# Performance work log

Hardware: AMD Instinct MI355X
Metric: run time of the kernel (lower is better)

## Reference

```python
import jax, jax.numpy as jnp
import numpy as np

H = 16                 # num_heads
BITS = (2, 4, 8)       # adaptive quantization precision options


def _adaptive_quant(t, labels):
    """t: [B,S,HD], labels: [B,S] int in {0,1,2}. Per-level masked min/max
    affine quantize-dequantize, matching AdaptiveQuantization.forward."""
    out = jnp.zeros_like(t)
    for level, bits in enumerate(BITS):
        m = (labels == level)[..., None]          # [B,S,1] broadcast over features
        qmax = float(2 ** bits - 1)
        tmin = jnp.min(jnp.where(m, t, jnp.inf))
        tmax = jnp.max(jnp.where(m, t, -jnp.inf))
        degen = (~jnp.isfinite(tmin)) | (~jnp.isfinite(tmax)) | (tmax == tmin)
        scale = jnp.where(degen, 1.0, (tmax - tmin) / qmax)
        zp = jnp.where(degen, 0.0, -tmin / scale)
        dq = (jnp.clip(jnp.round(t / scale + zp), 0.0, qmax) - zp) * scale
        out = jnp.where(m, dq, out)
    return out


def _importance(q, k, w_imp, b_imp, pm_f):
    """q,k: [B,H,S,D]; uses head 0 only, as in compute_importance_scores."""
    D = q.shape[-1]
    q0, k0 = q[:, 0], k[:, 0]                     # [B,S,D]
    attn = jax.nn.softmax(jnp.einsum('bsd,btd->bst', q0, k0) / np.sqrt(D), axis=-1)
    prompt_attn = attn @ pm_f                     # [B,S] sum over prompt keys
    bias = q0.mean(axis=1) @ w_imp + b_imp[0]     # [B]
    return prompt_attn + bias[:, None]            # [B,S]


def _split_heads(x, B, S, D):
    return x.reshape(B, S, H, D).transpose(0, 2, 1, 3)  # [B,H,S,D]


def _forward(hidden_states, Wq, Wk, Wv, Wo, w_imp, b_imp, prompt_mask, k_sel):
    B, S, HD = hidden_states.shape
    D = HD // H
    q = _split_heads(hidden_states @ Wq, B, S, D)
    k = _split_heads(hidden_states @ Wk, B, S, D)
    v = _split_heads(hidden_states @ Wv, B, S, D)
    pm_f = prompt_mask.astype(hidden_states.dtype)
    imp = _importance(q, k, w_imp, b_imp, pm_f)   # [B,S]
    # precision labels: >0.7 -> 2 ; 0.3..0.7 -> 1 ; else 0
    labels = jnp.where(imp > 0.7, 2, jnp.where(imp >= 0.3, 1, 0))
    ck = _adaptive_quant(k.transpose(0, 2, 1, 3).reshape(B, S, HD), labels)
    cv = _adaptive_quant(v.transpose(0, 2, 1, 3).reshape(B, S, HD), labels)
    ck = _split_heads(ck, B, S, D)
    cv = _split_heads(cv, B, S, D)
    if k_sel < S:  # top-k token gather along key/value sequence axis
        _, sel = jax.lax.top_k(imp, k_sel)        # [B,k_sel]
        idx = jnp.broadcast_to(sel[:, None, :, None], (B, H, k_sel, D))
        ck = jnp.take_along_axis(ck, idx, axis=2)
        cv = jnp.take_along_axis(cv, idx, axis=2)
    scores = jnp.einsum('bhsd,bhtd->bhst', q, ck) / np.sqrt(D)
    w = jax.nn.softmax(scores, axis=-1)
    out = jnp.einsum('bhst,bhtd->bhsd', w, cv)
    return out.transpose(0, 2, 1, 3).reshape(B, S, HD) @ Wo


def setup_inputs() -> dict:
    key = jax.random.key(0)
    ks = jax.random.split(key, 8)
    B, S, HD, D = 4, 2048, 1024, 64
    wscale = 2.0 / np.sqrt(HD)   # gives importance-softmax logits std ~4
    return {
        'hidden_states': jax.random.normal(ks[0], (B, S, HD), jnp.float32),
        'Wq': jax.random.normal(ks[1], (HD, HD), jnp.float32) * wscale,
        'Wk': jax.random.normal(ks[2], (HD, HD), jnp.float32) * wscale,
        'Wv': jax.random.normal(ks[3], (HD, HD), jnp.float32) * wscale,
        'Wo': jax.random.normal(ks[4], (HD, HD), jnp.float32) * wscale,
        'w_imp': jax.random.normal(ks[5], (D,), jnp.float32) * 0.02,
        'b_imp': jnp.zeros((1,), jnp.float32),
        'prompt_mask': jax.random.randint(ks[6], (S,), 0, 2).astype(bool),
    }


def reference(hidden_states, Wq, Wk, Wv, Wo, w_imp, b_imp, prompt_mask):
    B, S, HD = hidden_states.shape
    D = HD // H
    # pre-pass to get the (data-dependent, but concrete) selection count
    q = _split_heads(hidden_states @ Wq, B, S, D)
    k = _split_heads(hidden_states @ Wk, B, S, D)
    imp = _importance(q, k, w_imp, b_imp, prompt_mask.astype(hidden_states.dtype))
    thr = jnp.quantile(imp, 0.5)
    k_sel = int(jnp.max(jnp.sum(imp >= thr, axis=1)))
    return _forward(hidden_states, Wq, Wk, Wv, Wo, w_imp, b_imp, prompt_mask, k_sel)
```

## Files before the change

kernel.cpp:

```cpp
#include <hip/hip_runtime.h>
#include <hip/hip_bf16.h>
#include <math.h>

#define B_ 4
#define S_ 2048
#define H_ 16
#define D_ 64
#define HD_ 1024
#define NTOK 8192

#define NEGBIG (-3.0e38f)

typedef unsigned short u16;
typedef unsigned int u32;
typedef __attribute__((ext_vector_type(8))) short bf16x8;
typedef __attribute__((ext_vector_type(4))) float f32x4;
typedef __attribute__((ext_vector_type(4))) u16 u16x4;
typedef __attribute__((ext_vector_type(4))) u32 u32x4;

__device__ __forceinline__ float bf2f(u16 x){
  u32 u = ((u32)x) << 16; float f; __builtin_memcpy(&f, &u, 4); return f;
}
__device__ __forceinline__ u16 f2bf(float f){
  u32 u; __builtin_memcpy(&u, &f, 4);
  u32 r = (u + 0x7FFFu + ((u >> 16) & 1u)) >> 16;
  return (u16)r;
}
__device__ __forceinline__ void split3s(float v, u16 &h, u16 &m, u16 &l){
  h = f2bf(v); float r  = v - bf2f(h);
  m = f2bf(r); float r2 = r - bf2f(m);
  l = f2bf(r2);
}
__device__ __forceinline__ u32 fkey(float f){
  u32 u; __builtin_memcpy(&u, &f, 4);
  return (u & 0x80000000u) ? ~u : (u | 0x80000000u);
}
__device__ __forceinline__ float keyf(u32 k){
  u32 u = (k & 0x80000000u) ? (k & 0x7FFFFFFFu) : ~k;
  float f; __builtin_memcpy(&f, &u, 4); return f;
}
__device__ __forceinline__ void gload16(const u16* g, u16* l){
  __builtin_amdgcn_global_load_lds(
      (const __attribute__((address_space(1))) unsigned int*)g,
      (__attribute__((address_space(3))) unsigned int*)l, 16, 0, 0);
}

#define ST_KSEL 0
#define ST_KPAD 1
#define ST_NCK  2
#define ST_VKEY 4
#define ST_TIES 8
#define ST_MM   12
#define ST_BIAS 36

#define OFF_Q0   0ull
#define OFF_K    2097152ull
#define OFF_V    35651584ull
#define OFF_HS   69206016ull
#define OFF_WP   119537664ull
#define OFF_QB   134742016ull
#define OFF_IMP  151519232ull
#define OFF_LAB  151552000ull
#define OFF_SEL  151584768ull
#define OFF_ST   151617536ull
#define WS_NEED  151618560ull

#define WKH_O 0u
#define WKM_O 1048576u
#define WKL_O 2097152u
#define WVH_O 3145728u
#define WVM_O 4194304u
#define WVL_O 5242880u
#define WQH_O 6291456u
#define WQM_O 7340032u
#define WQL_O 7471104u
#define HSPL  8388608u

__global__ __launch_bounds__(256) void kt_split_h(const float* __restrict__ hid,
    u16* __restrict__ p0, u16* __restrict__ p1, u16* __restrict__ p2, u32* __restrict__ st){
  if (blockIdx.x == 0 && threadIdx.x < 12)
    st[ST_MM + threadIdx.x] = ((threadIdx.x % 6) < 3) ? 0xFFFFFFFFu : 0u;
  size_t i = (size_t)blockIdx.x*256 + threadIdx.x;
  float4 x = ((const float4*)hid)[i];
  u16 a0,a1,a2, b0,b1,b2, c0,c1,c2, d0,d1,d2;
  split3s(x.x, a0,a1,a2);
  split3s(x.y, b0,b1,b2);
  split3s(x.z, c0,c1,c2);
  split3s(x.w, d0,d1,d2);
  u16x4 v0 = {a0,b0,c0,d0};
  u16x4 v1 = {a1,b1,c1,d1};
  u16x4 v2 = {a2,b2,c2,d2};
  ((u16x4*)p0)[i] = v0;
  ((u16x4*)p1)[i] = v1;
  ((u16x4*)p2)[i] = v2;
}

__global__ __launch_bounds__(256) void kt_twts3(const float* __restrict__ Wk,
    const float* __restrict__ Wv, const float* __restrict__ Wq, u16* __restrict__ WP){
  int z = blockIdx.z;
  const float* Win = (z==0) ? Wk : (z==1) ? Wv : Wq;
  u16* wh = WP + ((z==0) ? WKH_O : (z==1) ? WVH_O : WQH_O);
  u16* wm = WP + ((z==0) ? WKM_O : (z==1) ? WVM_O : WQM_O);
  u16* wl = WP + ((z==0) ? WKL_O : (z==1) ? WVL_O : WQL_O);
  int mlrows = (z==2) ? 128 : 1024;
  __shared__ float t[32][33];
  int bx = blockIdx.x*32, by = blockIdx.y*32;
  int tx = threadIdx.x, ty = threadIdx.y;
  #pragma unroll
  for (int i=0;i<32;i+=8) t[ty+i][tx] = Win[(size_t)(by+ty+i)*HD_ + bx+tx];
  __syncthreads();
  #pragma unroll
  for (int i=0;i<32;i+=8){
    float v = t[tx][ty+i];
    int orow = bx+ty+i;
    u16 h,m,l;
    split3s(v,h,m,l);
    wh[(size_t)orow*HD_ + by+tx] = h;
    if (orow < mlrows){
      wm[(size_t)orow*HD_ + by+tx] = m;
      wl[(size_t)orow*HD_ + by+tx] = l;
    }
  }
}

__global__ __launch_bounds__(256) void kt_twto(const float* __restrict__ Win, u16* __restrict__ Wt){
  __shared__ float t[32][33];
  int bx = blockIdx.x*32, by = blockIdx.y*32;
  int tx = threadIdx.x, ty = threadIdx.y;
  #pragma unroll
  for (int i=0;i<32;i+=8) t[ty+i][tx] = Win[(size_t)(by+ty+i)*HD_ + bx+tx];
  __syncthreads();
  #pragma unroll
  for (int i=0;i<32;i+=8) Wt[(size_t)(bx+ty+i)*HD_ + by+tx] = f2bf(t[tx][ty+i]);
}

__global__ __launch_bounds__(256) void kt_gemm_kv1(const u16* __restrict__ HS,
    const u16* __restrict__ B0, const u16* __restrict__ B1, const u16* __restrict__ B2,
    float* __restrict__ Cf){
  int lin = blockIdx.x + (blockIdx.y << 3);
  int nl  = (lin & 7) * 64 + (lin >> 3);
  const int bx = nl & 7, by = nl >> 3;
  __shared__ u16 As0[128*32], As1[128*32], As2[128*32];
  __shared__ u16 Bs0[128*32], Bs1[128*32], Bs2[128*32];
  const int tid = threadIdx.x, lane = tid & 63;
  const int wid = tid >> 6, wr = wid >> 1, wc = wid & 1;
  const int m0 = by * 128, n0 = bx * 128;
  const int srow = lane & 15;
  const int sq   = (lane >> 4) << 3;
  const u16* gp[12];
  u16* lp[12];
  #pragma unroll
  for (int i = 0; i < 12; i++){
    int t = wid + 4*i, pl = t >> 3, g = t & 7;
    int row = g*16 + srow;
    const u16* base = (pl==0)? HS : (pl==1)? HS+HSPL : (pl==2)? HS+2u*HSPL
                     : (pl==3)? B0 : (pl==4)? B1 : B2;
    size_t roff = (pl < 3) ? (size_t)(m0+row)*HD_ : (size_t)(n0+row)*HD_;
    gp[i] = base + roff + sq;
    u16* lb = (pl==0)?As0:(pl==1)?As1:(pl==2)?As2:(pl==3)?Bs0:(pl==4)?Bs1:Bs2;
    lp[i] = lb + g*512;
  }
  f32x4 acc[4][4];
  #pragma unroll
  for (int i=0;i<4;i++)
    #pragma unroll
    for (int j=0;j<4;j++) acc[i][j] = (f32x4){0.f,0.f,0.f,0.f};
  for (int k0 = 0; k0 < HD_; k0 += 32){
    #pragma unroll
    for (int i = 0; i < 12; i++){ gload16(gp[i], lp[i]); gp[i] += 32; }
    __syncthreads();
    const int lro = lane*8;
    bf16x8 a0[4], a1[4], a2[4];
    #pragma unroll
    for (int i=0;i<4;i++){
      int ro = (wr*4 + i)*512 + lro;
      a0[i] = *(const bf16x8*)(As0 + ro);
      a1[i] = *(const bf16x8*)(As1 + ro);
      a2[i] = *(const bf16x8*)(As2 + ro);
    }
    #pragma unroll
    for (int j=0;j<4;j++){
      int co = (wc*4 + j)*512 + lro;
      bf16x8 b0 = *(const bf16x8*)(Bs0 + co);
      bf16x8 b1 = *(const bf16x8*)(Bs1 + co);
      bf16x8 b2 = *(const bf16x8*)(Bs2 + co);
      #pragma unroll
      for (int i=0;i<4;i++){
        acc[i][j] = __builtin_amdgcn_mfma_f32_16x16x32_bf16(a0[i], b0, acc[i][j], 0, 0, 0);
        acc[i][j] = __builtin_amdgcn_mfma_f32_16x16x32_bf16(a1[i], b0, acc[i][j], 0, 0, 0);
        acc[i][j] = __builtin_amdgcn_mfma_f32_16x16x32_bf16(a0[i], b1, acc[i][j], 0, 0, 0);
        acc[i][j] = __builtin_amdgcn_mfma_f32_16x16x32_bf16(a1[i], b1, acc[i][j], 0, 0, 0);
        acc[i][j] = __builtin_amdgcn_mfma_f32_16x16x32_bf16(a2[i], b0, acc[i][j], 0, 0, 0);
        acc[i][j] = __builtin_amdgcn_mfma_f32_16x16x32_bf16(a0[i], b2, acc[i][j], 0, 0, 0);
      }
    }
    __syncthreads();
  }
  const int row0 = m0 + wr*64, col0 = n0 + wc*64;
  #pragma unroll
  for (int i=0;i<4;i++)
    #pragma unroll
    for (int j=0;j<4;j++){
      int rr = row0 + i*16 + ((lane>>4)<<2);
      int cc = col0 + j*16 + (lane&15);
      #pragma unroll
      for (int r=0;r<4;r++)
        Cf[(size_t)(rr+r)*HD_ + cc] = acc[i][j][r];
    }
}

__global__ __launch_bounds__(256) void kt_gemm_q(const u16* __restrict__ HS, const u16* __restrict__ WP,
    u16* __restrict__ qb, float* __restrict__ q0){
  int lin = blockIdx.x + (blockIdx.y << 3);
  int nl  = (lin & 7) * 64 + (lin >> 3);
  const int bx = nl & 7, by = nl >> 3;
  const u16* B0 = WP+WQH_O;
  const u16* B1 = WP+WQM_O;
  const u16* B2 = WP+WQL_O;
  const bool full = (bx == 0);
  __shared__ u16 As0[128*32], As1[128*32], As2[128*32];
  __shared__ u16 Bs0[128*32], Bs1[128*32], Bs2[128*32];
  const int tid = threadIdx.x, lane = tid & 63;
  const int wid = tid >> 6, wr = wid >> 1, wc = wid & 1;
  const int m0 = by * 128, n0 = bx * 128;
  const int srow = lane & 15;
  const int sq   = (lane >> 4) << 3;
  const u16* gp[12];
  u16* lp[12];
  if (full){
    #pragma unroll
    for (int i = 0; i < 12; i++){
      int t = wid + 4*i, pl = t >> 3, g = t & 7;
      int row = g*16 + srow;
      const u16* base = (pl==0)? HS : (pl==1)? HS+HSPL : (pl==2)? HS+2u*HSPL
                       : (pl==3)? B0 : (pl==4)? B1 : B2;
      size_t roff = (pl < 3) ? (size_t)(m0+row)*HD_ : (size_t)(n0+row)*HD_;
      gp[i] = base + roff + sq;
      u16* lb = (pl==0)?As0:(pl==1)?As1:(pl==2)?As2:(pl==3)?Bs0:(pl==4)?Bs1:Bs2;
      lp[i] = lb + g*512;
    }
  } else {
    #pragma unroll
    for (int i = 0; i < 6; i++){
      int t = wid + 4*i, p3 = t >> 3, g = t & 7;
      int pl = (p3 == 2) ? 3 : p3;
      int row = g*16 + srow;
      const u16* base = (pl==0)? HS : (pl==1)? HS+HSPL : B0;
      size_t roff = (pl < 3) ? (size_t)(m0+row)*HD_ : (size_t)(n0+row)*HD_;
      gp[i] = base + roff + sq;
      u16* lb = (pl==0)?As0:(pl==1)?As1:Bs0;
      lp[i] = lb + g*512;
    }
  }
  f32x4 acc[4][4];
  #pragma unroll
  for (int i=0;i<4;i++)
    #pragma unroll
    for (int j=0;j<4;j++) acc[i][j] = (f32x4){0.f,0.f,0.f,0.f};
  for (int k0 = 0; k0 < HD_; k0 += 32){
    if (full){
      #pragma unroll
      for (int i = 0; i < 12; i++){ gload16(gp[i], lp[i]); gp[i] += 32; }
    } else {
      #pragma unroll
      for (int i = 0; i < 6; i++){ gload16(gp[i], lp[i]); gp[i] += 32; }
    }
    __syncthreads();
    const int lro = lane*8;
    bf16x8 a0[4], a1[4], a2[4];
    #pragma unroll
    for (int i=0;i<4;i++){
      int ro = (wr*4 + i)*512 + lro;
      a0[i] = *(const bf16x8*)(As0 + ro);
      a1[i] = *(const bf16x8*)(As1 + ro);
      if (full) a2[i] = *(const bf16x8*)(As2 + ro);
    }
    #pragma unroll
    for (int j=0;j<4;j++){
      int co = (wc*4 + j)*512 + lro;
      bf16x8 b0 = *(const bf16x8*)(Bs0 + co);
      if (full){
        bf16x8 b1 = *(const bf16x8*)(Bs1 + co);
        bf16x8 b2 = *(const bf16x8*)(Bs2 + co);
        #pragma unroll
        for (int i=0;i<4;i++){
          acc[i][j] = __builtin_amdgcn_mfma_f32_16x16x32_bf16(a0[i], b0, acc[i][j], 0, 0, 0);
          acc[i][j] = __builtin_amdgcn_mfma_f32_16x16x32_bf16(a1[i], b0, acc[i][j], 0, 0, 0);
          acc[i][j] = __builtin_amdgcn_mfma_f32_16x16x32_bf16(a0[i], b1, acc[i][j], 0, 0, 0);
          acc[i][j] = __builtin_amdgcn_mfma_f32_16x16x32_bf16(a1[i], b1, acc[i][j], 0, 0, 0);
          acc[i][j] = __builtin_amdgcn_mfma_f32_16x16x32_bf16(a2[i], b0, acc[i][j], 0, 0, 0);
          acc[i][j] = __builtin_amdgcn_mfma_f32_16x16x32_bf16(a0[i], b2, acc[i][j], 0, 0, 0);
        }
      } else {
        #pragma unroll
        for (int i=0;i<4;i++){
          acc[i][j] = __builtin_amdgcn_mfma_f32_16x16x32_bf16(a0[i], b0, acc[i][j], 0, 0, 0);
          acc[i][j] = __builtin_amdgcn_mfma_f32_16x16x32_bf16(a1[i], b0, acc[i][j], 0, 0, 0);
        }
      }
    }
    __syncthreads();
  }
  const int row0 = m0 + wr*64, col0 = n0 + wc*64;
  #pragma unroll
  for (int i=0;i<4;i++)
    #pragma unroll
    for (int j=0;j<4;j++){
      int rr = row0 + i*16 + ((lane>>4)<<2);
      int cc = col0 + j*16 + (lane&15);
      #pragma unroll
      for (int r=0;r<4;r++){
        float v = acc[i][j][r];
        qb[(size_t)(rr+r)*HD_ + cc] = f2bf(v);
        if (cc < 64) q0[(size_t)(rr+r)*64 + cc] = v;
      }
    }
}

__global__ __launch_bounds__(256) void kt_gemm_o(const u16* __restrict__ A, const u16* __restrict__ Bt,
    float* __restrict__ out){
  int lin = blockIdx.x + (blockIdx.y << 3);
  int nl  = (lin & 7) * 64 + (lin >> 3);
  const int bx = nl & 7, by = nl >> 3;
  __shared__ u16 As[128*32];
  __shared__ u16 Bs[128*32];
  const int tid = threadIdx.x, lane = tid & 63;
  const int wid = tid >> 6, wr = wid >> 1, wc = wid & 1;
  const int m0 = by * 128, n0 = bx * 128;
  const u16* gp[4];
  u16* lp[4];
  #pragma unroll
  for (int i = 0; i < 4; i++){
    int t = wid + 4*i, pl = t >> 3, g = t & 7;
    int row = g*16 + (lane & 15);
    gp[i] = (pl ? (Bt + (size_t)(n0+row)*HD_) : (A + (size_t)(m0+row)*HD_)) + ((lane>>4)<<3);
    lp[i] = (pl ? Bs : As) + g*512;
  }
  f32x4 acc[4][4];
  #pragma unroll
  for (int i=0;i<4;i++)
    #pragma unroll
    for (int j=0;j<4;j++) acc[i][j] = (f32x4){0.f,0.f,0.f,0.f};
  for (int k0 = 0; k0 < HD_; k0 += 32){
    #pragma unroll
    for (int i = 0; i < 4; i++){ gload16(gp[i], lp[i]); gp[i] += 32; }
    __syncthreads();
    const int lro = lane*8;
    bf16x8 af[4], bg[4];
    #pragma unroll
    for (int i=0;i<4;i++){
      af[i] = *(const bf16x8*)(As + (wr*4 + i)*512 + lro);
      bg[i] = *(const bf16x8*)(Bs + (wc*4 + i)*512 + lro);
    }
    #pragma unroll
    for (int i=0;i<4;i++)
      #pragma unroll
      for (int j=0;j<4;j++)
        acc[i][j] = __builtin_amdgcn_mfma_f32_16x16x32_bf16(af[i], bg[j], acc[i][j], 0, 0, 0);
    __syncthreads();
  }
  const int row0 = m0 + wr*64, col0 = n0 + wc*64;
  #pragma unroll
  for (int i=0;i<4;i++)
    #pragma unroll
    for (int j=0;j<4;j++){
      int rr = row0 + i*16 + ((lane>>4)<<2);
      int cc = col0 + j*16 + (lane&15);
      #pragma unroll
      for (int r=0;r<4;r++)
        out[(size_t)(rr+r)*HD_ + cc] = acc[i][j][r];
    }
}

__global__ __launch_bounds__(256) void kt_k0t(const float* __restrict__ Kf, float* __restrict__ k0t){
  __shared__ float t[32][33];
  int b = blockIdx.z, s0 = blockIdx.x*32, d0 = blockIdx.y*32;
  int tx = threadIdx.x, ty = threadIdx.y;
  #pragma unroll
  for (int i=0;i<32;i+=8) t[ty+i][tx] = Kf[((size_t)b*S_ + s0+ty+i)*HD_ + d0+tx];
  __syncthreads();
  #pragma unroll
  for (int i=0;i<32;i+=8) k0t[((size_t)b*D_ + d0+ty+i)*S_ + s0+tx] = t[tx][ty+i];
}

__global__ __launch_bounds__(1024) void kt_bias(const float* __restrict__ q0, const float* __restrict__ wimp,
    const float* __restrict__ bimp, u32* __restrict__ st){
  int b = blockIdx.x;
  int d = threadIdx.x & 63, sg = threadIdx.x >> 6;
  float acc = 0.f;
  for (int s = sg; s < S_; s += 16) acc += q0[((size_t)b*S_ + s)*64 + d];
  __shared__ float red[16][64];
  red[sg][d] = acc;
  __syncthreads();
  if (sg == 0){
    float tot = 0.f;
    #pragma unroll
    for (int i=0;i<16;i++) tot += red[i][d];
    float term = (tot / (float)S_) * wimp[d];
    #pragma unroll
    for (int off=32; off; off>>=1) term += __shfl_xor(term, off);
    if (d == 0) ((float*)st)[ST_BIAS + b] = term + bimp[0];
  }
}

__global__ __launch_bounds__(256) void kt_imp(const float* __restrict__ q0, const float* __restrict__ k0t,
    const int* __restrict__ pm, const u32* __restrict__ st, float* __restrict__ imp){
  int b = blockIdx.y, r0 = blockIdx.x * 16;
  int tid = threadIdx.x, lane = tid & 63, w = tid >> 6;
  __shared__ float qs[16][64];
  __shared__ float pms[S_];
  __shared__ int mode8;
  if (tid == 0) mode8 = 0;
  __syncthreads();
  const unsigned char* pmb = (const unsigned char*)pm;
  int flag = 0;
  for (int i = tid; i < S_; i += 256) if (i & 3) flag |= pmb[i];
  if (flag) atomicOr(&mode8, 1);
  for (int i = tid; i < 16*64; i += 256){
    int rr = i >> 6, dd = i & 63;
    qs[rr][dd] = q0[((size_t)b*S_ + r0 + rr)*64 + dd];
  }
  __syncthreads();
  if (mode8){ for (int i = tid; i < S_; i += 256) pms[i] = pmb[i] ? 1.f : 0.f; }
  else      { for (int i = tid; i < S_; i += 256) pms[i] = pm[i]  ? 1.f : 0.f; }
  __syncthreads();
  float sc[4][32];
  #pragma unroll
  for (int r=0;r<4;r++)
    #pragma unroll
    for (int j=0;j<32;j++) sc[r][j] = 0.f;
  const float* kb = k0t + (size_t)b*D_*S_;
  for (int d=0; d<64; d++){
    const float* krow = kb + (size_t)d*S_;
    float kx[32];
    #pragma unroll
    for (int j=0;j<32;j++) kx[j] = krow[lane + 64*j];
    #pragma unroll
    for (int r=0;r<4;r++){
      float qd = qs[w*4 + r][d];
      #pragma unroll
      for (int j=0;j<32;j++) sc[r][j] = fmaf(qd, kx[j], sc[r][j]);
    }
  }
  float bias = ((const float*)st)[ST_BIAS + b];
  #pragma unroll
  for (int r=0;r<4;r++){
    float mx = NEGBIG;
    #pragma unroll
    for (int j=0;j<32;j++) mx = fmaxf(mx, sc[r][j]);
    #pragma unroll
    for (int off=32; off; off>>=1) mx = fmaxf(mx, __shfl_xor(mx, off));
    mx *= 0.125f;
    float se = 0.f, sp = 0.f;
    #pragma unroll
    for (int j=0;j<32;j++){
      float e = expf(sc[r][j]*0.125f - mx);
      se += e;
      sp += e * pms[lane + 64*j];
    }
    #pragma unroll
    for (int off=32; off; off>>=1){ se += __shfl_xor(se, off); sp += __shfl_xor(sp, off); }
    if (lane == 0) imp[(size_t)b*S_ + r0 + w*4 + r] = sp/se + bias;
  }
}

__global__ __launch_bounds__(1024) void kt_stats(const float* __restrict__ imp, u32* __restrict__ st){
  __shared__ u32 keys[NTOK];
  __shared__ u32 res2[2];
  __shared__ int cnts[4];
  int tid = threadIdx.x, lane = tid & 63, w = tid >> 6;
  for (int i = tid; i < NTOK; i += 1024) keys[i] = fkey(imp[i]);
  __syncthreads();
  if (w < 2){
    int kk = 4095 + w;
    u32 lo = 0u, hi = 0xFFFFFFFFu;
    while (lo < hi){
      u32 mid = lo + ((hi - lo) >> 1);
      int c = 0;
      for (int i = lane; i < NTOK; i += 64) c += (keys[i] <= mid) ? 1 : 0;
      #pragma unroll
      for (int off=32; off; off>>=1) c += __shfl_xor(c, off);
      if (c >= kk + 1) hi = mid; else lo = mid + 1;
    }
    if (lane == 0) res2[w] = lo;
  }
  __syncthreads();
  float a = keyf(res2[0]), bq = keyf(res2[1]);
  float thr = __fadd_rn(a, __fmul_rn(__fsub_rn(bq, a), 0.5f));
  u32 tkey = fkey(thr);
  if (w < 4){
    int c = 0;
    for (int i = lane; i < S_; i += 64) c += (keys[w*S_ + i] >= tkey) ? 1 : 0;
    #pragma unroll
    for (int off=32; off; off>>=1) c += __shfl_xor(c, off);
    if (lane == 0) cnts[w] = c;
  }
  __syncthreads();
  int ksel = max(max(cnts[0], cnts[1]), max(cnts[2], cnts[3]));
  if (tid == 0){
    int kpad = (ksel + 63) & ~63;
    ((int*)st)[ST_KSEL] = ksel;
    ((int*)st)[ST_KPAD] = kpad;
    ((int*)st)[ST_NCK]  = kpad >> 6;
  }
  if (w < 4){
    int kk = S_ - ksel;
    u32 lo = 0u, hi = 0xFFFFFFFFu;
    while (lo < hi){
      u32 mid = lo + ((hi - lo) >> 1);
      int c = 0;
      for (int i = lane; i < S_; i += 64) c += (keys[w*S_ + i] <= mid) ? 1 : 0;
      #pragma unroll
      for (int off=32; off; off>>=1) c += __shfl_xor(c, off);
      if (c >= kk + 1) hi = mid; else lo = mid + 1;
    }
    int cle = 0;
    for (int i = lane; i < S_; i += 64) cle += (keys[w*S_ + i] <= lo) ? 1 : 0;
    #pragma unroll
    for (int off=32; off; off>>=1) cle += __shfl_xor(cle, off);
    if (lane == 0){
      st[ST_VKEY + w] = lo;
      ((int*)st)[ST_TIES + w] = ksel - (S_ - cle);
    }
  }
}

__global__ __launch_bounds__(1024) void kt_select(const float* __restrict__ imp, const u32* __restrict__ st,
    int* __restrict__ sel, u32* __restrict__ lab){
  int b = blockIdx.x, tid = threadIdx.x, lane = tid & 63, w = tid >> 6;
  u32 vkey = st[ST_VKEY + b];
  int ties = ((const int*)st)[ST_TIES + b];
  int s0 = tid*2, s1 = s0 + 1;
  float f0 = imp[(size_t)b*S_ + s0], f1 = imp[(size_t)b*S_ + s1];
  lab[(size_t)b*S_ + s0] = (f0 > 0.7f) ? 2u : ((f0 >= 0.3f) ? 1u : 0u);
  lab[(size_t)b*S_ + s1] = (f1 > 0.7f) ? 2u : ((f1 >= 0.3f) ? 1u : 0u);
  u32 k0 = fkey(f0), k1 = fkey(f1);
  int g0 = (k0 > vkey), g1 = (k1 > vkey);
  int t0 = (k0 == vkey), t1 = (k1 == vkey);
  __shared__ int wtot[16];
  int tsum = t0 + t1, incl = tsum;
  #pragma unroll
  for (int off=1; off<64; off<<=1){ int nv = __shfl_up(incl, off); if (lane >= off) incl += nv; }
  if (lane == 63) wtot[w] = incl;
  __syncthreads();
  int woff = 0;
  for (int i=0;i<w;i++) woff += wtot[i];
  int tie0 = woff + incl - tsum;
  int tie1 = tie0 + t0;
  int sf0 = g0 | (t0 & ((tie0 < ties) ? 1 : 0));
  int sf1 = g1 | (t1 & ((tie1 < ties) ? 1 : 0));
  __syncthreads();
  int ssum = sf0 + sf1; incl = ssum;
  #pragma unroll
  for (int off=1; off<64; off<<=1){ int nv = __shfl_up(incl, off); if (lane >= off) incl += nv; }
  if (lane == 63) wtot[w] = incl;
  __syncthreads();
  woff = 0;
  for (int i=0;i<w;i++) woff += wtot[i];
  int p0 = woff + incl - ssum;
  if (sf0) sel[(size_t)b*S_ + p0] = s0;
  if (sf1) sel[(size_t)b*S_ + p0 + sf0] = s1;
}

__global__ __launch_bounds__(256) void kt_minmax(const float* __restrict__ Kf, const float* __restrict__ Vf,
    const u32* __restrict__ lab, u32* __restrict__ st){
  u32 mn[6], mx[6];
  #pragma unroll
  for (int q=0;q<6;q++){ mn[q] = 0xFFFFFFFFu; mx[q] = 0u; }
  const int n4 = NTOK * HD_ / 4;
  for (int i = blockIdx.x*blockDim.x + threadIdx.x; i < n4; i += gridDim.x*blockDim.x){
    u32 l = min(lab[i >> 8], 2u);
    float4 kv = ((const float4*)Kf)[i];
    float4 vv = ((const float4*)Vf)[i];
    u32 a0=fkey(kv.x), a1=fkey(kv.y), a2=fkey(kv.z), a3=fkey(kv.w);
    u32 klo = min(min(a0,a1),min(a2,a3)), khi = max(max(a0,a1),max(a2,a3));
    if (klo < mn[l]) mn[l] = klo;
    if (khi > mx[l]) mx[l] = khi;
    u32 b0=fkey(vv.x), b1=fkey(vv.y), b2=fkey(vv.z), b3=fkey(vv.w);
    u32 vlo = min(min(b0,b1),min(b2,b3)), vhi = max(max(b0,b1),max(b2,b3));
    if (vlo < mn[3+l]) mn[3+l] = vlo;
    if (vhi > mx[3+l]) mx[3+l] = vhi;
  }
  #pragma unroll
  for (int q=0;q<6;q++){
    #pragma unroll
    for (int off=32; off; off>>=1){
      u32 om = (u32)__shfl_xor((int)mn[q], off); if (om < mn[q]) mn[q] = om;
      u32 oM = (u32)__shfl_xor((int)mx[q], off); if (oM > mx[q]) mx[q] = oM;
    }
  }
  __shared__ u32 smn[4][6], smx[4][6];
  int lane = threadIdx.x & 63, w = threadIdx.x >> 6;
  if (lane == 0){
    #pragma unroll
    for (int q=0;q<6;q++){ smn[w][q]=mn[q]; smx[w][q]=mx[q]; }
  }
  __syncthreads();
  if (threadIdx.x < 6){
    int q = threadIdx.x;
    u32 m = smn[0][q], M = smx[0][q];
    #pragma unroll
    for (int i=1;i<4;i++){ if (smn[i][q] < m) m = smn[i][q]; if (smx[i][q] > M) M = smx[i][q]; }
    int minSlot = ST_MM + ((q < 3) ? q : q + 3);
    atomicMin(&st[minSlot], m);
    atomicMax(&st[minSlot + 3], M);
  }
}

__device__ __forceinline__ void scales_for(const u32* st, u32 l, float &qmx,
    float &sK, float &zK, float &sV, float &zV){
  qmx = (l==0) ? 3.f : (l==1) ? 15.f : 255.f;
  u32 mnk = st[ST_MM + l], mxk = st[ST_MM + 3 + l];
  sK = 1.f; zK = 0.f;
  if (!(mnk == 0xFFFFFFFFu || mxk == 0u)){
    float tmn = keyf(mnk), tmx = keyf(mxk);
    if (tmx != tmn){ sK = __fdiv_rn(__fsub_rn(tmx, tmn), qmx); zK = __fdiv_rn(-tmn, sK); }
  }
  u32 mnv = st[ST_MM + 6 + l], mxv = st[ST_MM + 9 + l];
  sV = 1.f; zV = 0.f;
  if (!(mnv == 0xFFFFFFFFu || mxv == 0u)){
    float tmn = keyf(mnv), tmx = keyf(mxv);
    if (tmx != tmn){ sV = __fdiv_rn(__fsub_rn(tmx, tmn), qmx); zV = __fdiv_rn(-tmn, sV); }
  }
}

__device__ __forceinline__ float dqz(float x, float s, float z, float q){
  float t = rintf(__fadd_rn(__fdiv_rn(x, s), z));
  t = fminf(fmaxf(t, 0.f), q);
  return __fmul_rn(__fsub_rn(t, z), s);
}

__global__ __launch_bounds__(256) void kt_buildck(const float* __restrict__ Kf, const float* __restrict__ Vf,
    const int* __restrict__ sel, const u32* __restrict__ lab, const u32* __restrict__ st,
    u16* __restrict__ ckh, u16* __restrict__ ckl, u16* __restrict__ cvb){
  int b = blockIdx.z, j = blockIdx.y;
  int ksel = ((const int*)st)[ST_KSEL], kpad = ((const int*)st)[ST_KPAD];
  if (j >= kpad) return;
  int dd = threadIdx.x * 4;
  size_t oo = ((size_t)b*S_ + j)*HD_ + dd;
  if (j >= ksel){
    u16x4 z4 = {0,0,0,0};
    *(u16x4*)(ckh + oo) = z4;
    *(u16x4*)(ckl + oo) = z4;
    *(u16x4*)(cvb + oo) = z4;
    return;
  }
  int s = sel[(size_t)b*S_ + j];
  u32 l = min(lab[(size_t)b*S_ + s], 2u);
  float qmx, sK, zK, sV, zV;
  scales_for(st, l, qmx, sK, zK, sV, zV);
  float4 kv = *(const float4*)(Kf + ((size_t)b*S_ + s)*HD_ + dd);
  float4 vv = *(const float4*)(Vf + ((size_t)b*S_ + s)*HD_ + dd);
  float kd0 = dqz(kv.x,sK,zK,qmx), kd1 = dqz(kv.y,sK,zK,qmx), kd2 = dqz(kv.z,sK,zK,qmx), kd3 = dqz(kv.w,sK,zK,qmx);
  u16 h0 = f2bf(kd0), h1 = f2bf(kd1), h2 = f2bf(kd2), h3 = f2bf(kd3);
  u16x4 kh = {h0, h1, h2, h3};
  u16x4 kl = {f2bf(kd0 - bf2f(h0)), f2bf(kd1 - bf2f(h1)), f2bf(kd2 - bf2f(h2)), f2bf(kd3 - bf2f(h3))};
  u16x4 vo = {f2bf(dqz(vv.x,sV,zV,qmx)), f2bf(dqz(vv.y,sV,zV,qmx)),
              f2bf(dqz(vv.z,sV,zV,qmx)), f2bf(dqz(vv.w,sV,zV,qmx))};
  *(u16x4*)(ckh + oo) = kh;
  *(u16x4*)(ckl + oo) = kl;
  *(u16x4*)(cvb + oo) = vo;
}

__global__ __launch_bounds__(256) void kt_cvt(const u16* __restrict__ cvb, u16* __restrict__ cvT,
    const u32* __restrict__ st){
  int kpad = ((const int*)st)[ST_KPAD];
  int j0 = blockIdx.x*32;
  if (j0 >= kpad) return;
  int d0 = blockIdx.y*32, b = blockIdx.z;
  __shared__ u16 t[32][33];
  int tx = threadIdx.x, ty = threadIdx.y;
  #pragma unroll
  for (int i=0;i<32;i+=8) t[ty+i][tx] = cvb[((size_t)b*S_ + j0+ty+i)*HD_ + d0+tx];
  __syncthreads();
  #pragma unroll
  for (int i=0;i<32;i+=8) cvT[((size_t)b*HD_ + d0+ty+i)*S_ + j0+tx] = t[tx][ty+i];
}

#define ATTN_QSTEP(KSH, KSL, VS, QA0, QA1, MRUN, LRUN, OARR)                       \
  {                                                                                \
    f32x4 sc[4];                                                                   \
    const int fro = ((lane>>3)&1)*512 + (((lane>>4)*8 + (lane&7))<<3);             \
    __builtin_amdgcn_s_setprio(1);                                                 \
    _Pragma("unroll")                                                              \
    for (int nt=0; nt<4; nt++){                                                    \
      int ro = nt*1024 + fro;                                                      \
      bf16x8 bh0 = *(const bf16x8*)(KSH + ro);                                     \
      bf16x8 bh1 = *(const bf16x8*)(KSH + ro + 256);                               \
      bf16x8 bl0 = *(const bf16x8*)(KSL + ro);                                     \
      bf16x8 bl1 = *(const bf16x8*)(KSL + ro + 256);                               \
      f32x4 zzv = (f32x4){0.f,0.f,0.f,0.f};                                        \
      zzv = __builtin_amdgcn_mfma_f32_16x16x32_bf16(QA0, bh0, zzv, 0, 0, 0);       \
      zzv = __builtin_amdgcn_mfma_f32_16x16x32_bf16(QA1, bh1, zzv, 0, 0, 0);       \
      zzv = __builtin_amdgcn_mfma_f32_16x16x32_bf16(QA0, bl0, zzv, 0, 0, 0);       \
      zzv = __builtin_amdgcn_mfma_f32_16x16x32_bf16(QA1, bl1, zzv, 0, 0, 0);       \
      sc[nt] = zzv;                                                                \
    }                                                                              \
    __builtin_amdgcn_s_setprio(0);                                                 \
    float cm[4] = {NEGBIG,NEGBIG,NEGBIG,NEGBIG};                                   \
    _Pragma("unroll")                                                              \
    for (int nt=0; nt<4; nt++){                                                    \
      int tg = c*64 + nt*16 + (lane&15);                                           \
      bool valid = (tg < ksel);                                                    \
      _Pragma("unroll")                                                            \
      for (int r=0;r<4;r++){                                                       \
        float x = valid ? sc[nt][r]*0.125f : NEGBIG;                               \
        sc[nt][r] = x;                                                             \
        cm[r] = fmaxf(cm[r], x);                                                   \
      }                                                                            \
    }                                                                              \
    _Pragma("unroll")                                                              \
    for (int r=0;r<4;r++){                                                         \
      _Pragma("unroll")                                                            \
      for (int off=1; off<16; off<<=1) cm[r] = fmaxf(cm[r], __shfl_xor(cm[r], off));\
    }                                                                              \
    float alpha[4], rs[4];                                                         \
    _Pragma("unroll")                                                              \
    for (int r=0;r<4;r++){                                                         \
      float mn = fmaxf(MRUN[r], cm[r]);                                            \
      alpha[r] = __expf(MRUN[r] - mn);                                             \
      MRUN[r] = mn;                                                                \
      rs[r] = 0.f;                                                                 \
    }                                                                              \
    _Pragma("unroll")                                                              \
    for (int nt=0; nt<4; nt++)                                                     \
      _Pragma("unroll")                                                            \
      for (int r=0;r<4;r++){                                                       \
        float p = __expf(sc[nt][r] - MRUN[r]);                                     \
        sc[nt][r] = p;                                                             \
        rs[r] += p;                                                                \
      }                                                                            \
    _Pragma("unroll")                                                              \
    for (int r=0;r<4;r++){                                                         \
      _Pragma("unroll")                                                            \
      for (int off=1; off<16; off<<=1) rs[r] += __shfl_xor(rs[r], off);            \
      LRUN[r] = LRUN[r]*alpha[r] + rs[r];                                          \
    }                                                                              \
    _Pragma("unroll")                                                              \
    for (int dt=0; dt<4; dt++)                                                     \
      _Pragma("unroll")                                                            \
      for (int r=0;r<4;r++) OARR[dt][r] *= alpha[r];                               \
    _Pragma("unroll")                                                              \
    for (int nt=0; nt<4; nt++)                                                     \
      _Pragma("unroll")                                                            \
      for (int r=0;r<4;r++){                                                       \
        float p = sc[nt][r];                                                       \
        u16 ph = f2bf(p);                                                          \
        int o2 = (((lane>>4)<<2) + r)*72 + nt*16 + (lane&15);                      \
        pwh[o2] = ph;                                                              \
        pwl[o2] = f2bf(p - bf2f(ph));                                              \
      }                                                                            \
    bf16x8 pa0h = *(const bf16x8*)(pwh + (lane&15)*72 + ((lane>>4)<<3));           \
    bf16x8 pa1h = *(const bf16x8*)(pwh + (lane&15)*72 + 32 + ((lane>>4)<<3));      \
    bf16x8 pa0l = *(const bf16x8*)(pwl + (lane&15)*72 + ((lane>>4)<<3));           \
    bf16x8 pa1l = *(const bf16x8*)(pwl + (lane&15)*72 + 32 + ((lane>>4)<<3));      \
    __builtin_amdgcn_s_setprio(1);                                                 \
    _Pragma("unroll")                                                              \
    for (int dt=0; dt<4; dt++){                                                    \
      int vo = dt*1024 + fro;                                                      \
      bf16x8 v0 = *(const bf16x8*)(VS + vo);                                       \
      bf16x8 v1 = *(const bf16x8*)(VS + vo + 256);                                 \
      OARR[dt] = __builtin_amdgcn_mfma_f32_16x16x32_bf16(pa0h, v0, OARR[dt], 0, 0, 0);\
      OARR[dt] = __builtin_amdgcn_mfma_f32_16x16x32_bf16(pa1h, v1, OARR[dt], 0, 0, 0);\
      OARR[dt] = __builtin_amdgcn_mfma_f32_16x16x32_bf16(pa0l, v0, OARR[dt], 0, 0, 0);\
      OARR[dt] = __builtin_amdgcn_mfma_f32_16x16x32_bf16(pa1l, v1, OARR[dt], 0, 0, 0);\
    }                                                                              \
    __builtin_amdgcn_s_setprio(0);                                                 \
  }

__global__ __launch_bounds__(256) void kt_attn(const u16* __restrict__ qb, const u16* __restrict__ ckh,
    const u16* __restrict__ ckl, const u16* __restrict__ cvT, const u32* __restrict__ st,
    u16* __restrict__ ao){
  int m0 = blockIdx.x * 128, h = blockIdx.y, b = blockIdx.z;
  int ksel = ((const int*)st)[ST_KSEL], nck = ((const int*)st)[ST_NCK];
  int tid = threadIdx.x, lane = tid & 63, w = tid >> 6;
  __shared__ u16 cksh[2*4096];
  __shared__ u16 cksl[2*4096];
  __shared__ u16 cvs[2*4096];
  __shared__ u16 psh[4][16*72];
  __shared__ u16 psl[4][16*72];
  const u16* gp[6];
  u16* lp[6];
  int adv[6];
  #pragma unroll
  for (int i = 0; i < 6; i++){
    int t = w + 4*i, pl = t >> 3, g = t & 7;
    if (pl == 0){
      gp[i] = ckh + ((size_t)b*S_ + g*8 + (lane&7))*HD_ + h*64 + ((lane>>3)<<3);
      lp[i] = cksh + g*512;
      adv[i] = 64*HD_;
    } else if (pl == 1){
      gp[i] = ckl + ((size_t)b*S_ + g*8 + (lane&7))*HD_ + h*64 + ((lane>>3)<<3);
      lp[i] = cksl + g*512;
      adv[i] = 64*HD_;
    } else {
      gp[i] = cvT + ((size_t)b*HD_ + h*64 + g*8 + (lane&7))*S_ + ((lane>>3)<<3);
      lp[i] = cvs + g*512;
      adv[i] = 64;
    }
  }
  const u16* qrow0 = qb + ((size_t)b*S_ + m0      + w*16 + (lane&15))*HD_ + h*64;
  const u16* qrow1 = qb + ((size_t)b*S_ + m0 + 64 + w*16 + (lane&15))*HD_ + h*64;
  bf16x8 q0a = *(const bf16x8*)(qrow0 + ((lane>>4)<<3));
  bf16x8 q0b = *(const bf16x8*)(qrow0 + 32 + ((lane>>4)<<3));
  bf16x8 q1a = *(const bf16x8*)(qrow1 + ((lane>>4)<<3));
  bf16x8 q1b = *(const bf16x8*)(qrow1 + 32 + ((lane>>4)<<3));
  f32x4 o0[4], o1[4];
  #pragma unroll
  for (int dt=0; dt<4; dt++){ o0[dt] = (f32x4){0.f,0.f,0.f,0.f}; o1[dt] = (f32x4){0.f,0.f,0.f,0.f}; }
  float m0r[4] = {NEGBIG,NEGBIG,NEGBIG,NEGBIG};
  float m1r[4] = {NEGBIG,NEGBIG,NEGBIG,NEGBIG};
  float l0r[4] = {0.f,0.f,0.f,0.f};
  float l1r[4] = {0.f,0.f,0.f,0.f};
  u16* pwh = &psh[w][0];
  u16* pwl = &psl[w][0];
  #pragma unroll
  for (int i = 0; i < 6; i++){ gload16(gp[i], lp[i]); gp[i] += adv[i]; }
  __syncthreads();
  for (int c = 0; c < nck; c++){
    int cur = c & 1, nxt = cur ^ 1;
    if (c + 1 < nck){
      #pragma unroll
      for (int i = 0; i < 6; i++){ gload16(gp[i], lp[i] + nxt*4096); gp[i] += adv[i]; }
    }
    const u16* ksh = cksh + cur*4096;
    const u16* ksl = cksl + cur*4096;
    const u16* vs  = cvs  + cur*4096;
    ATTN_QSTEP(ksh, ksl, vs, q0a, q0b, m0r, l0r, o0)
    ATTN_QSTEP(ksh, ksl, vs, q1a, q1b, m1r, l1r, o1)
    __syncthreads();
  }
  #pragma unroll
  for (int dt=0; dt<4; dt++)
    #pragma unroll
    for (int r=0;r<4;r++){
      int dd = dt*16 + (lane&15);
      int row0 = m0 + w*16 + ((lane>>4)<<2) + r;
      float v0 = o0[dt][r] / fmaxf(l0r[r], 1e-37f);
      ao[((size_t)b*S_ + row0)*HD_ + h*64 + dd] = f2bf(v0);
      int row1 = row0 + 64;
      float v1 = o1[dt][r] / fmaxf(l1r[r], 1e-37f);
      ao[((size_t)b*S_ + row1)*HD_ + h*64 + dd] = f2bf(v1);
    }
}

extern "C" void kernel_launch(void* const* d_in, const int* in_sizes, int n_in,
                              void* d_out, int out_size, void* d_ws, size_t ws_size,
                              hipStream_t stream){
  if (ws_size < WS_NEED) return;
  const float* hid  = (const float*)d_in[0];
  const float* Wq   = (const float*)d_in[1];
  const float* Wk   = (const float*)d_in[2];
  const float* Wv   = (const float*)d_in[3];
  const float* Wo   = (const float*)d_in[4];
  const float* wimp = (const float*)d_in[5];
  const float* bimp = (const float*)d_in[6];
  const int*   pm   = (const int*)d_in[7];

  char* ws = (char*)d_ws;
  float* Q0  = (float*)(ws + OFF_Q0);
  float* Kf  = (float*)(ws + OFF_K);
  float* Vf  = (float*)(ws + OFF_V);
  u16*   HS  = (u16*)(ws + OFF_HS);
  u16*   WP  = (u16*)(ws + OFF_WP);
  u16*   QB  = (u16*)(ws + OFF_QB);
  float* IMP = (float*)(ws + OFF_IMP);
  u32*   LAB = (u32*)(ws + OFF_LAB);
  int*   SEL = (int*)(ws + OFF_SEL);
  u32*   ST  = (u32*)(ws + OFF_ST);
  float* K0T = (float*)(ws + OFF_HS);
  u16*   CKH = (u16*)(ws + OFF_HS);
  u16*   CKL = (u16*)(ws + OFF_HS + 16777216ull);
  u16*   CVB = (u16*)(ws + OFF_HS + 33554432ull);
  u16*   CVT = (u16*)(ws + OFF_V);
  u16*   AO  = (u16*)(ws + OFF_K);
  u16*   WOT = (u16*)(ws + OFF_Q0);

  dim3 tb32(32, 8);
  kt_split_h<<<8192, 256, 0, stream>>>(hid, HS, HS + HSPL, HS + 2u*HSPL, ST);
  kt_twts3<<<dim3(32,32,3), tb32, 0, stream>>>(Wk, Wv, Wq, WP);
  kt_gemm_kv1<<<dim3(8,64), 256, 0, stream>>>(HS, WP+WKH_O, WP+WKM_O, WP+WKL_O, Kf);
  kt_gemm_kv1<<<dim3(8,64), 256, 0, stream>>>(HS, WP+WVH_O, WP+WVM_O, WP+WVL_O, Vf);
  kt_gemm_q<<<dim3(8,64), 256, 0, stream>>>(HS, WP, QB, Q0);
  kt_k0t<<<dim3(64,2,4), tb32, 0, stream>>>(Kf, K0T);
  kt_bias<<<4, 1024, 0, stream>>>(Q0, wimp, bimp, ST);
  kt_imp<<<dim3(128,4), 256, 0, stream>>>(Q0, K0T, pm, ST, IMP);
  kt_stats<<<1, 1024, 0, stream>>>(IMP, ST);
  kt_select<<<4, 1024, 0, stream>>>(IMP, ST, SEL, LAB);
  kt_minmax<<<256, 256, 0, stream>>>(Kf, Vf, LAB, ST);
  kt_buildck<<<dim3(1,2048,4), 256, 0, stream>>>(Kf, Vf, SEL, LAB, ST, CKH, CKL, CVB);
  kt_cvt<<<dim3(64,32,4), tb32, 0, stream>>>(CVB, CVT, ST);
  kt_attn<<<dim3(16,16,4), 256, 0, stream>>>(QB, CKH, CKL, CVT, ST, AO);
  kt_twto<<<dim3(32,32), tb32, 0, stream>>>(Wo, WOT);
  kt_gemm_o<<<dim3(8,64), 256, 0, stream>>>(AO, WOT, (float*)d_out);
}
```

Before: 696.5 us.

## Single-buffer attention K/V tiles and skip masking on full chunks

The attention kernel's double-buffered LDS staging of K-hi, K-lo and V tiles becomes a single buffer, halving that shared memory, so each chunk now loads and then synchronises before computing. Full chunks (below ksel/64) take a specialised path that drops the per-element validity test. The smaller LDS footprint may allow more resident blocks per CU. In exchange, global-load latency is no longer overlapped with MFMA work inside a block.

```diff
diff --git a/kernel.cpp b/kernel.cpp
--- a/kernel.cpp
+++ b/kernel.cpp
@@ -677,7 +677,7 @@
   for (int i=0;i<32;i+=8) cvT[((size_t)b*HD_ + d0+ty+i)*S_ + j0+tx] = t[tx][ty+i];
 }
 
-#define ATTN_QSTEP(KSH, KSL, VS, QA0, QA1, MRUN, LRUN, OARR)                       \
+#define ATTN_QSTEP(QA0, QA1, MRUN, LRUN, OARR, MASKQ)                              \
   {                                                                                \
     f32x4 sc[4];                                                                   \
     const int fro = ((lane>>3)&1)*512 + (((lane>>4)*8 + (lane&7))<<3);             \
@@ -685,10 +685,10 @@
     _Pragma("unroll")                                                              \
     for (int nt=0; nt<4; nt++){                                                    \
       int ro = nt*1024 + fro;                                                      \
-      bf16x8 bh0 = *(const bf16x8*)(KSH + ro);                                     \
-      bf16x8 bh1 = *(const bf16x8*)(KSH + ro + 256);                               \
-      bf16x8 bl0 = *(const bf16x8*)(KSL + ro);                                     \
-      bf16x8 bl1 = *(const bf16x8*)(KSL + ro + 256);                               \
+      bf16x8 bh0 = *(const bf16x8*)(cksh + ro);                                    \
+      bf16x8 bh1 = *(const bf16x8*)(cksh + ro + 256);                              \
+      bf16x8 bl0 = *(const bf16x8*)(cksl + ro);                                    \
+      bf16x8 bl1 = *(const bf16x8*)(cksl + ro + 256);                              \
       f32x4 zzv = (f32x4){0.f,0.f,0.f,0.f};                                        \
       zzv = __builtin_amdgcn_mfma_f32_16x16x32_bf16(QA0, bh0, zzv, 0, 0, 0);       \
       zzv = __builtin_amdgcn_mfma_f32_16x16x32_bf16(QA1, bh1, zzv, 0, 0, 0);       \
@@ -700,8 +700,7 @@
     float cm[4] = {NEGBIG,NEGBIG,NEGBIG,NEGBIG};                                   \
     _Pragma("unroll")                                                              \
     for (int nt=0; nt<4; nt++){                                                    \
-      int tg = c*64 + nt*16 + (lane&15);                                           \
-      bool valid = (tg < ksel);                                                    \
+      bool valid = MASKQ ? ((c*64 + nt*16 + (lane&15)) < ksel) : true;             \
       _Pragma("unroll")                                                            \
       for (int r=0;r<4;r++){                                                       \
         float x = valid ? sc[nt][r]*0.125f : NEGBIG;                               \
@@ -758,8 +757,8 @@
     _Pragma("unroll")                                                              \
     for (int dt=0; dt<4; dt++){                                                    \
       int vo = dt*1024 + fro;                                                      \
-      bf16x8 v0 = *(const bf16x8*)(VS + vo);                                       \
-      bf16x8 v1 = *(const bf16x8*)(VS + vo + 256);                                 \
+      bf16x8 v0 = *(const bf16x8*)(cvs + vo);                                      \
+      bf16x8 v1 = *(const bf16x8*)(cvs + vo + 256);                                \
       OARR[dt] = __builtin_amdgcn_mfma_f32_16x16x32_bf16(pa0h, v0, OARR[dt], 0, 0, 0);\
       OARR[dt] = __builtin_amdgcn_mfma_f32_16x16x32_bf16(pa1h, v1, OARR[dt], 0, 0, 0);\
       OARR[dt] = __builtin_amdgcn_mfma_f32_16x16x32_bf16(pa0l, v0, OARR[dt], 0, 0, 0);\
@@ -774,9 +773,9 @@
   int m0 = blockIdx.x * 128, h = blockIdx.y, b = blockIdx.z;
   int ksel = ((const int*)st)[ST_KSEL], nck = ((const int*)st)[ST_NCK];
   int tid = threadIdx.x, lane = tid & 63, w = tid >> 6;
-  __shared__ u16 cksh[2*4096];
-  __shared__ u16 cksl[2*4096];
-  __shared__ u16 cvs[2*4096];
+  __shared__ u16 cksh[4096];
+  __shared__ u16 cksl[4096];
+  __shared__ u16 cvs[4096];
   __shared__ u16 psh[4][16*72];
   __shared__ u16 psl[4][16*72];
   const u16* gp[6];
@@ -814,20 +813,18 @@
   float l1r[4] = {0.f,0.f,0.f,0.f};
   u16* pwh = &psh[w][0];
   u16* pwl = &psl[w][0];
-  #pragma unroll
-  for (int i = 0; i < 6; i++){ gload16(gp[i], lp[i]); gp[i] += adv[i]; }
-  __syncthreads();
+  const int nfull = ksel >> 6;
   for (int c = 0; c < nck; c++){
-    int cur = c & 1, nxt = cur ^ 1;
-    if (c + 1 < nck){
-      #pragma unroll
-      for (int i = 0; i < 6; i++){ gload16(gp[i], lp[i] + nxt*4096); gp[i] += adv[i]; }
-    }
-    const u16* ksh = cksh + cur*4096;
-    const u16* ksl = cksl + cur*4096;
-    const u16* vs  = cvs  + cur*4096;
-    ATTN_QSTEP(ksh, ksl, vs, q0a, q0b, m0r, l0r, o0)
-    ATTN_QSTEP(ksh, ksl, vs, q1a, q1b, m1r, l1r, o1)
+    #pragma unroll
+    for (int i = 0; i < 6; i++){ gload16(gp[i], lp[i]); gp[i] += adv[i]; }
+    __syncthreads();
+    if (c < nfull){
+      ATTN_QSTEP(q0a, q0b, m0r, l0r, o0, 0)
+      ATTN_QSTEP(q1a, q1b, m1r, l1r, o1, 0)
+    } else {
+      ATTN_QSTEP(q0a, q0b, m0r, l0r, o0, 1)
+      ATTN_QSTEP(q1a, q1b, m1r, l1r, o1, 1)
+    }
     __syncthreads();
   }
   #pragma unroll
```

After: 713.7 us. 1.02x slower.
